# Kernel tuning notes

Hardware: AMD Instinct MI355X
Metric: run time of the kernel (lower is better)

## Reference

```python
import jax, jax.numpy as jnp
import numpy as np

N_NODES = 100000
N_EDGES = 600000
D_IN = 128
D_OUT = 128


def setup_inputs() -> dict:
    key = jax.random.key(0)
    ks = jax.random.split(key, 8)
    stdv = 1.0 / np.sqrt(D_OUT)
    return {
        "x": jax.random.normal(ks[0], (N_NODES, D_IN), dtype=jnp.float32),
        "edge_src": jax.random.randint(ks[1], (N_EDGES,), 0, N_NODES, dtype=jnp.int32),
        "edge_dst": jax.random.randint(ks[2], (N_EDGES,), 0, N_NODES, dtype=jnp.int32),
        "edge_weight": jax.random.uniform(ks[3], (N_EDGES,), dtype=jnp.float32),
        "weight_l": jax.random.uniform(ks[4], (D_IN, D_OUT), minval=-stdv, maxval=stdv, dtype=jnp.float32),
        "bias_l": jax.random.uniform(ks[5], (D_OUT,), minval=-stdv, maxval=stdv, dtype=jnp.float32),
        "weight_r": jax.random.uniform(ks[6], (D_IN, D_OUT), minval=-stdv, maxval=stdv, dtype=jnp.float32),
        "bias_r": jax.random.uniform(ks[7], (D_OUT,), minval=-stdv, maxval=stdv, dtype=jnp.float32),
    }


def reference(x, edge_src, edge_dst, edge_weight, weight_l, bias_l, weight_r, bias_r):
    # h = input @ weight_l  -> [N, D_OUT]
    h = x @ weight_l
    # spmm(adj, h): out[dst] += adj[dst, src] * h[src]
    msgs = h[edge_src] * edge_weight[:, None]          # [E, D_OUT] gather
    agg = jax.ops.segment_sum(msgs, edge_dst, num_segments=N_NODES)
    out = agg + bias_l
    # root_weight branch (size is None)
    out = out + x @ weight_r + bias_r
    return out
```

## Files before the change

kernel.cpp:

```cpp
#include <hip/hip_runtime.h>
#include <hip/hip_bf16.h>

#define D 128
#define SCAN_BLK 256
#define SCAN_VPT 4
#define SCAN_TILE (SCAN_BLK * SCAN_VPT)

typedef __attribute__((ext_vector_type(8))) short short8;
typedef __attribute__((ext_vector_type(4))) float f32x4;

__global__ __launch_bounds__(256) void prep_w(
    const float* __restrict__ Wl, const float* __restrict__ Wr,
    const float* __restrict__ bl, const float* __restrict__ br,
    __hip_bfloat16* __restrict__ WTl, __hip_bfloat16* __restrict__ WTr,
    float* __restrict__ bsum) {
  const int tid = blockIdx.x * 256 + threadIdx.x;
  const int n = (tid >> 7) & 127;
  const int k = tid & 127;
  if (tid < 16384) {
    WTl[n * D + k] = __float2bfloat16(Wl[k * D + n]);
  } else {
    WTr[n * D + k] = __float2bfloat16(Wr[k * D + n]);
  }
  if (tid < 128) bsum[tid] = bl[tid] + br[tid];
}

__global__ __launch_bounds__(256) void gemm_h(
    const float* __restrict__ x, const __hip_bfloat16* __restrict__ WTl,
    __hip_bfloat16* __restrict__ h,
    const int* __restrict__ edst, int* __restrict__ deg, int n_edges,
    int n_rowtiles) {
  const int gsz = gridDim.x * 256;
  for (int e = blockIdx.x * 256 + threadIdx.x; e < n_edges; e += gsz)
    atomicAdd(&deg[edst[e]], 1);

  __shared__ __hip_bfloat16 xs[16][136];
  const int t = threadIdx.x;
  const int wave = t >> 6;
  const int lane = t & 63;
  const int m = lane & 15;
  const int q = lane >> 4;

  short8 bfrag[2][4];
#pragma unroll
  for (int c = 0; c < 2; ++c) {
    const int n0 = wave * 32 + c * 16;
#pragma unroll
    for (int ks = 0; ks < 4; ++ks)
      bfrag[c][ks] = *(const short8*)&WTl[(n0 + m) * D + ks * 32 + q * 8];
  }

  const int srow = t >> 4;
  const int scol = (t & 15) * 8;

  for (int rt = blockIdx.x; rt < n_rowtiles; rt += gridDim.x) {
    const int rowbase = rt * 16;
    {
      const float4* src = (const float4*)&x[(size_t)(rowbase + srow) * D + scol];
      const float4 v0 = src[0], v1 = src[1];
      __hip_bfloat16* dst = &xs[srow][scol];
      dst[0] = __float2bfloat16(v0.x); dst[1] = __float2bfloat16(v0.y);
      dst[2] = __float2bfloat16(v0.z); dst[3] = __float2bfloat16(v0.w);
      dst[4] = __float2bfloat16(v1.x); dst[5] = __float2bfloat16(v1.y);
      dst[6] = __float2bfloat16(v1.z); dst[7] = __float2bfloat16(v1.w);
    }
    __syncthreads();

    f32x4 acc[2];
#pragma unroll
    for (int c = 0; c < 2; ++c)
#pragma unroll
      for (int r = 0; r < 4; ++r) acc[c][r] = 0.f;

#pragma unroll
    for (int ks = 0; ks < 4; ++ks) {
      const short8 afrag = *(const short8*)&xs[m][ks * 32 + q * 8];
#pragma unroll
      for (int c = 0; c < 2; ++c)
        acc[c] = __builtin_amdgcn_mfma_f32_16x16x32_bf16(afrag, bfrag[c][ks], acc[c], 0, 0, 0);
    }

#pragma unroll
    for (int c = 0; c < 2; ++c) {
      const int n = wave * 32 + c * 16 + m;
#pragma unroll
      for (int r = 0; r < 4; ++r)
        h[(size_t)(rowbase + q * 4 + r) * D + n] = __float2bfloat16(acc[c][r]);
    }
    __syncthreads();
  }
}

__global__ __launch_bounds__(SCAN_BLK) void scan1_kernel(
    const int* __restrict__ deg, int* __restrict__ offsets,
    int* __restrict__ partials, int n) {
  __shared__ int sdata[SCAN_BLK];
  const int t = threadIdx.x;
  const int base = blockIdx.x * SCAN_TILE + t * SCAN_VPT;

  int v[SCAN_VPT];
  int s = 0;
#pragma unroll
  for (int j = 0; j < SCAN_VPT; ++j) {
    v[j] = (base + j < n) ? deg[base + j] : 0;
    s += v[j];
  }
  sdata[t] = s;
  __syncthreads();
  for (int off = 1; off < SCAN_BLK; off <<= 1) {
    int xv = (t >= off) ? sdata[t - off] : 0;
    __syncthreads();
    sdata[t] += xv;
    __syncthreads();
  }
  int excl = sdata[t] - s;
  if (t == SCAN_BLK - 1) partials[blockIdx.x] = sdata[t];
  int run = excl;
#pragma unroll
  for (int j = 0; j < SCAN_VPT; ++j) {
    if (base + j < n) offsets[base + j] = run;
    run += v[j];
  }
}

__global__ __launch_bounds__(SCAN_BLK) void scan3_kernel(
    int* __restrict__ offsets, int* __restrict__ pos,
    const int* __restrict__ partials, int n, int n_edges) {
  __shared__ int s_add;
  const int t = threadIdx.x;
  if (t < 64) {
    int v = 0;
    for (int j = t; j < blockIdx.x; j += 64) v += partials[j];
#pragma unroll
    for (int off = 32; off > 0; off >>= 1) v += __shfl_down(v, off);
    if (t == 0) s_add = v;
  }
  __syncthreads();
  const int add = s_add;
  const int base = blockIdx.x * SCAN_TILE + t * SCAN_VPT;
#pragma unroll
  for (int j = 0; j < SCAN_VPT; ++j) {
    const int i = base + j;
    if (i < n) {
      const int o = offsets[i] + add;
      offsets[i] = o;
      pos[i] = o;
    }
  }
  if (blockIdx.x == 0 && t == 0) offsets[n] = n_edges;
}

__global__ __launch_bounds__(256) void scatter_kernel(
    const int* __restrict__ esrc, const int* __restrict__ edst,
    const float* __restrict__ ew, int* __restrict__ pos,
    int2* __restrict__ pairs, int n_edges) {
  const int e = blockIdx.x * 256 + threadIdx.x;
  if (e >= n_edges) return;
  const int d = edst[e];
  const int slot = atomicAdd(&pos[d], 1);
  pairs[slot] = make_int2(esrc[e], __float_as_int(ew[e]));
}

__global__ __launch_bounds__(256) void sage_out(
    const float* __restrict__ x, const __hip_bfloat16* __restrict__ WTr,
    const float* __restrict__ bsum, const __hip_bfloat16* __restrict__ h,
    const int* __restrict__ offsets, const int2* __restrict__ pairs,
    float* __restrict__ out) {
  __shared__ __hip_bfloat16 xs[16][136];
  __shared__ float ot[16][D];
  const int t = threadIdx.x;
  const int wave = t >> 6;
  const int lane = t & 63;
  const int m = lane & 15;
  const int q = lane >> 4;
  const int rowbase = blockIdx.x * 16;

  short8 bfrag[2][4];
#pragma unroll
  for (int c = 0; c < 2; ++c) {
    const int n0 = wave * 32 + c * 16;
#pragma unroll
    for (int ks = 0; ks < 4; ++ks)
      bfrag[c][ks] = *(const short8*)&WTr[(n0 + m) * D + ks * 32 + q * 8];
  }

  {
    const int srow = t >> 4;
    const int scol = (t & 15) * 8;
    const float4* src = (const float4*)&x[(size_t)(rowbase + srow) * D + scol];
    const float4 v0 = src[0], v1 = src[1];
    __hip_bfloat16* dst = &xs[srow][scol];
    dst[0] = __float2bfloat16(v0.x); dst[1] = __float2bfloat16(v0.y);
    dst[2] = __float2bfloat16(v0.z); dst[3] = __float2bfloat16(v0.w);
    dst[4] = __float2bfloat16(v1.x); dst[5] = __float2bfloat16(v1.y);
    dst[6] = __float2bfloat16(v1.z); dst[7] = __float2bfloat16(v1.w);
  }
  __syncthreads();

  f32x4 acc[2];
#pragma unroll
  for (int c = 0; c < 2; ++c)
#pragma unroll
    for (int r = 0; r < 4; ++r) acc[c][r] = 0.f;

#pragma unroll
  for (int ks = 0; ks < 4; ++ks) {
    const short8 afrag = *(const short8*)&xs[m][ks * 32 + q * 8];
#pragma unroll
    for (int c = 0; c < 2; ++c)
      acc[c] = __builtin_amdgcn_mfma_f32_16x16x32_bf16(afrag, bfrag[c][ks], acc[c], 0, 0, 0);
  }

#pragma unroll
  for (int c = 0; c < 2; ++c) {
    const int n = wave * 32 + c * 16 + m;
    const float b = bsum[n];
#pragma unroll
    for (int r = 0; r < 4; ++r)
      ot[q * 4 + r][n] = acc[c][r] + b;
  }
  __syncthreads();

  const __hip_bfloat162* __restrict__ h2 = (const __hip_bfloat162*)h;
#pragma unroll
  for (int j = 0; j < 4; ++j) {
    const int ln = wave * 4 + j;
    const int node = rowbase + ln;
    const int begin = offsets[node];
    const int end = offsets[node + 1];

    float2 a = *(const float2*)&ot[ln][2 * lane];

    int i = begin;
    for (; i + 4 <= end; i += 4) {
      const int2 p0 = pairs[i + 0];
      const int2 p1 = pairs[i + 1];
      const int2 p2 = pairs[i + 2];
      const int2 p3 = pairs[i + 3];
      const __hip_bfloat162 a0 = h2[(size_t)p0.x * (D / 2) + lane];
      const __hip_bfloat162 a1 = h2[(size_t)p1.x * (D / 2) + lane];
      const __hip_bfloat162 a2 = h2[(size_t)p2.x * (D / 2) + lane];
      const __hip_bfloat162 a3 = h2[(size_t)p3.x * (D / 2) + lane];
      const float w0 = __int_as_float(p0.y), w1 = __int_as_float(p1.y);
      const float w2 = __int_as_float(p2.y), w3 = __int_as_float(p3.y);
      a.x = fmaf(w0, __bfloat162float(a0.x), a.x);
      a.y = fmaf(w0, __bfloat162float(a0.y), a.y);
      a.x = fmaf(w1, __bfloat162float(a1.x), a.x);
      a.y = fmaf(w1, __bfloat162float(a1.y), a.y);
      a.x = fmaf(w2, __bfloat162float(a2.x), a.x);
      a.y = fmaf(w2, __bfloat162float(a2.y), a.y);
      a.x = fmaf(w3, __bfloat162float(a3.x), a.x);
      a.y = fmaf(w3, __bfloat162float(a3.y), a.y);
    }
    for (; i < end; ++i) {
      const int2 p = pairs[i];
      const __hip_bfloat162 av = h2[(size_t)p.x * (D / 2) + lane];
      const float w = __int_as_float(p.y);
      a.x = fmaf(w, __bfloat162float(av.x), a.x);
      a.y = fmaf(w, __bfloat162float(av.y), a.y);
    }
    *(float2*)&out[(size_t)node * D + 2 * lane] = a;
  }
}

extern "C" void kernel_launch(void* const* d_in, const int* in_sizes, int n_in,
                              void* d_out, int out_size, void* d_ws, size_t ws_size,
                              hipStream_t stream) {
  const float* x   = (const float*)d_in[0];
  const int* esrc  = (const int*)d_in[1];
  const int* edst  = (const int*)d_in[2];
  const float* ew  = (const float*)d_in[3];
  const float* Wl  = (const float*)d_in[4];
  const float* bl  = (const float*)d_in[5];
  const float* Wr  = (const float*)d_in[6];
  const float* br  = (const float*)d_in[7];
  float* out = (float*)d_out;

  const int n_nodes = in_sizes[0] / D;
  const int n_edges = in_sizes[1];

  char* ws = (char*)d_ws;
  size_t off = 0;
  __hip_bfloat16* h = (__hip_bfloat16*)(ws + off);
  off += (size_t)n_nodes * D * sizeof(__hip_bfloat16);
  off = (off + 15) & ~15ull;
  int* offsets = (int*)(ws + off);
  off += (size_t)(n_nodes + 1) * sizeof(int);
  off = (off + 15) & ~15ull;
  int* pos = (int*)(ws + off);
  off += (size_t)n_nodes * sizeof(int);
  off = (off + 15) & ~15ull;
  int* partials = (int*)(ws + off);
  off += 1024 * sizeof(int);
  off = (off + 15) & ~15ull;
  int2* pairs = (int2*)(ws + off);
  off += (size_t)n_edges * sizeof(int2);
  off = (off + 15) & ~15ull;
  __hip_bfloat16* WTl = (__hip_bfloat16*)(ws + off);
  off += (size_t)D * D * sizeof(__hip_bfloat16);
  __hip_bfloat16* WTr = (__hip_bfloat16*)(ws + off);
  off += (size_t)D * D * sizeof(__hip_bfloat16);
  float* bsum = (float*)(ws + off);
  off += D * sizeof(float);

  const int n_rowtiles = (n_nodes + 15) / 16;

  hipMemsetAsync(pos, 0, (size_t)n_nodes * sizeof(int), stream);
  prep_w<<<128, 256, 0, stream>>>(Wl, Wr, bl, br, WTl, WTr, bsum);

  const int gemm_grid = n_rowtiles < 2048 ? n_rowtiles : 2048;
  gemm_h<<<gemm_grid, 256, 0, stream>>>(x, WTl, h, edst, pos, n_edges, n_rowtiles);

  const int nparts = (n_nodes + SCAN_TILE - 1) / SCAN_TILE;
  scan1_kernel<<<nparts, SCAN_BLK, 0, stream>>>(pos, offsets, partials, n_nodes);
  scan3_kernel<<<nparts, SCAN_BLK, 0, stream>>>(offsets, pos, partials, n_nodes, n_edges);
  scatter_kernel<<<(n_edges + 255) / 256, 256, 0, stream>>>(esrc, edst, ew, pos, pairs, n_edges);

  sage_out<<<n_rowtiles, 256, 0, stream>>>(x, WTr, bsum, h, offsets, pairs, out);
}
```

Baseline: 236.9 us.

## Stage block's neighbor rows into LDS with cooperative gathers issued before the GEMM

The sage_out kernel now gathers the h rows of all edges belonging to its 16-node block cooperatively into shared memory, in chunks of 112 edges. Each thread loads 64 bytes of a row with int4 loads, and the first chunk's loads are issued before the x@Wr MFMA section so their latency overlaps with the GEMM. Each wave then accumulates its 4 nodes from LDS and adds the root/bias term at the end. This replaces the per-wave serial 4-byte-per-lane gathers with wider, more parallel memory requests. In exchange it uses about 30KB of LDS, adds extra barriers for high-degree blocks, and sets a launch-bounds occupancy hint of 4.

```diff
diff --git a/kernel.cpp b/kernel.cpp
--- a/kernel.cpp
+++ b/kernel.cpp
@@ -5,6 +5,9 @@
 #define SCAN_BLK 256
 #define SCAN_VPT 4
 #define SCAN_TILE (SCAN_BLK * SCAN_VPT)
+
+#define KC 112
+#define HROW 272
 
 typedef __attribute__((ext_vector_type(8))) short short8;
 typedef __attribute__((ext_vector_type(4))) float f32x4;
@@ -161,13 +164,16 @@
   pairs[slot] = make_int2(esrc[e], __float_as_int(ew[e]));
 }
 
-__global__ __launch_bounds__(256) void sage_out(
+__global__ __launch_bounds__(256, 4) void sage_out(
     const float* __restrict__ x, const __hip_bfloat16* __restrict__ WTr,
     const float* __restrict__ bsum, const __hip_bfloat16* __restrict__ h,
     const int* __restrict__ offsets, const int2* __restrict__ pairs,
     float* __restrict__ out) {
-  __shared__ __hip_bfloat16 xs[16][136];
   __shared__ float ot[16][D];
+  __shared__ float wbuf[KC];
+  __shared__ __align__(16) char Hbuf[KC * HROW];
+  __hip_bfloat16 (*xs)[136] = reinterpret_cast<__hip_bfloat16(*)[136]>(Hbuf);
+
   const int t = threadIdx.x;
   const int wave = t >> 6;
   const int lane = t & 63;
@@ -175,6 +181,36 @@
   const int q = lane >> 4;
   const int rowbase = blockIdx.x * 16;
 
+  const int gB0 = offsets[rowbase];
+  const int Eb = offsets[rowbase + 16] - gB0;
+  int nb[4], ne[4];
+#pragma unroll
+  for (int j = 0; j < 4; ++j) {
+    nb[j] = offsets[rowbase + wave * 4 + j] - gB0;
+    ne[j] = offsets[rowbase + wave * 4 + j + 1] - gB0;
+  }
+
+  const int cnt0 = Eb < KC ? Eb : KC;
+  const int le0 = t >> 2;
+  const int le1 = (t + 256) >> 2;
+  const int qt = t & 3;
+  const bool v0 = le0 < cnt0;
+  const bool v1 = le1 < cnt0;
+  int2 pr0 = make_int2(0, 0), pr1 = make_int2(0, 0);
+  int4 g0[4], g1[4];
+  if (v0) {
+    pr0 = pairs[gB0 + le0];
+    const int4* p = (const int4*)((const char*)h + ((size_t)(unsigned)pr0.x << 8) + (qt << 6));
+#pragma unroll
+    for (int i = 0; i < 4; ++i) g0[i] = p[i];
+  }
+  if (v1) {
+    pr1 = pairs[gB0 + le1];
+    const int4* p = (const int4*)((const char*)h + ((size_t)(unsigned)pr1.x << 8) + (qt << 6));
+#pragma unroll
+    for (int i = 0; i < 4; ++i) g1[i] = p[i];
+  }
+
   short8 bfrag[2][4];
 #pragma unroll
   for (int c = 0; c < 2; ++c) {
@@ -188,12 +224,12 @@
     const int srow = t >> 4;
     const int scol = (t & 15) * 8;
     const float4* src = (const float4*)&x[(size_t)(rowbase + srow) * D + scol];
-    const float4 v0 = src[0], v1 = src[1];
+    const float4 v0f = src[0], v1f = src[1];
     __hip_bfloat16* dst = &xs[srow][scol];
-    dst[0] = __float2bfloat16(v0.x); dst[1] = __float2bfloat16(v0.y);
-    dst[2] = __float2bfloat16(v0.z); dst[3] = __float2bfloat16(v0.w);
-    dst[4] = __float2bfloat16(v1.x); dst[5] = __float2bfloat16(v1.y);
-    dst[6] = __float2bfloat16(v1.z); dst[7] = __float2bfloat16(v1.w);
+    dst[0] = __float2bfloat16(v0f.x); dst[1] = __float2bfloat16(v0f.y);
+    dst[2] = __float2bfloat16(v0f.z); dst[3] = __float2bfloat16(v0f.w);
+    dst[4] = __float2bfloat16(v1f.x); dst[5] = __float2bfloat16(v1f.y);
+    dst[6] = __float2bfloat16(v1f.z); dst[7] = __float2bfloat16(v1f.w);
   }
   __syncthreads();
 
@@ -221,45 +257,75 @@
   }
   __syncthreads();
 
-  const __hip_bfloat162* __restrict__ h2 = (const __hip_bfloat162*)h;
+  float2 a[4];
+#pragma unroll
+  for (int j = 0; j < 4; ++j) a[j] = make_float2(0.f, 0.f);
+
+  for (int base = 0; base < Eb; base += KC) {
+    const int cnt = (Eb - base) < KC ? (Eb - base) : KC;
+    if (base == 0) {
+      if (v0) {
+        char* dst = &Hbuf[le0 * HROW + (qt << 6)];
+#pragma unroll
+        for (int i = 0; i < 4; ++i) ((int4*)dst)[i] = g0[i];
+        if (qt == 0) wbuf[le0] = __int_as_float(pr0.y);
+      }
+      if (v1) {
+        char* dst = &Hbuf[le1 * HROW + (qt << 6)];
+#pragma unroll
+        for (int i = 0; i < 4; ++i) ((int4*)dst)[i] = g1[i];
+        if (qt == 0) wbuf[le1] = __int_as_float(pr1.y);
+      }
+    } else {
+      __syncthreads();
+#pragma unroll
+      for (int s = 0; s < 2; ++s) {
+        const int le = (t + s * 256) >> 2;
+        if (le < cnt) {
+          const int2 pr = pairs[gB0 + base + le];
+          const int4* p = (const int4*)((const char*)h + ((size_t)(unsigned)pr.x << 8) + (qt << 6));
+          int4 g[4];
+#pragma unroll
+          for (int i = 0; i < 4; ++i) g[i] = p[i];
+          char* dst = &Hbuf[le * HROW + (qt << 6)];
+#pragma unroll
+          for (int i = 0; i < 4; ++i) ((int4*)dst)[i] = g[i];
+          if (qt == 0) wbuf[le] = __int_as_float(pr.y);
+        }
+      }
+    }
+    __syncthreads();
+
+#pragma unroll
+    for (int j = 0; j < 4; ++j) {
+      const int lo = nb[j] > base ? nb[j] : base;
+      const int hi0 = base + cnt;
+      const int hi = ne[j] < hi0 ? ne[j] : hi0;
+      if (lo < hi) {
+        int li = lo - base;
+        float w = wbuf[li];
+        __hip_bfloat162 hv = *(const __hip_bfloat162*)&Hbuf[li * HROW + lane * 4];
+        for (int i = lo + 1; i < hi; ++i) {
+          const int lj = i - base;
+          const float nw = wbuf[lj];
+          const __hip_bfloat162 nv = *(const __hip_bfloat162*)&Hbuf[lj * HROW + lane * 4];
+          a[j].x = fmaf(w, __bfloat162float(hv.x), a[j].x);
+          a[j].y = fmaf(w, __bfloat162float(hv.y), a[j].y);
+          w = nw; hv = nv;
+        }
+        a[j].x = fmaf(w, __bfloat162float(hv.x), a[j].x);
+        a[j].y = fmaf(w, __bfloat162float(hv.y), a[j].y);
+      }
+    }
+  }
+
 #pragma unroll
   for (int j = 0; j < 4; ++j) {
     const int ln = wave * 4 + j;
-    const int node = rowbase + ln;
-    const int begin = offsets[node];
-    const int end = offsets[node + 1];
-
-    float2 a = *(const float2*)&ot[ln][2 * lane];
-
-    int i = begin;
-    for (; i + 4 <= end; i += 4) {
-      const int2 p0 = pairs[i + 0];
-      const int2 p1 = pairs[i + 1];
-      const int2 p2 = pairs[i + 2];
-      const int2 p3 = pairs[i + 3];
-      const __hip_bfloat162 a0 = h2[(size_t)p0.x * (D / 2) + lane];
-      const __hip_bfloat162 a1 = h2[(size_t)p1.x * (D / 2) + lane];
-      const __hip_bfloat162 a2 = h2[(size_t)p2.x * (D / 2) + lane];
-      const __hip_bfloat162 a3 = h2[(size_t)p3.x * (D / 2) + lane];
-      const float w0 = __int_as_float(p0.y), w1 = __int_as_float(p1.y);
-      const float w2 = __int_as_float(p2.y), w3 = __int_as_float(p3.y);
-      a.x = fmaf(w0, __bfloat162float(a0.x), a.x);
-      a.y = fmaf(w0, __bfloat162float(a0.y), a.y);
-      a.x = fmaf(w1, __bfloat162float(a1.x), a.x);
-      a.y = fmaf(w1, __bfloat162float(a1.y), a.y);
-      a.x = fmaf(w2, __bfloat162float(a2.x), a.x);
-      a.y = fmaf(w2, __bfloat162float(a2.y), a.y);
-      a.x = fmaf(w3, __bfloat162float(a3.x), a.x);
-      a.y = fmaf(w3, __bfloat162float(a3.y), a.y);
-    }
-    for (; i < end; ++i) {
-      const int2 p = pairs[i];
-      const __hip_bfloat162 av = h2[(size_t)p.x * (D / 2) + lane];
-      const float w = __int_as_float(p.y);
-      a.x = fmaf(w, __bfloat162float(av.x), a.x);
-      a.y = fmaf(w, __bfloat162float(av.y), a.y);
-    }
-    *(float2*)&out[(size_t)node * D + 2 * lane] = a;
+    float2 o = *(const float2*)&ot[ln][2 * lane];
+    o.x += a[j].x;
+    o.y += a[j].y;
+    *(float2*)&out[(size_t)(rowbase + ln) * D + 2 * lane] = o;
   }
 }
 
```

Measured after the change: 269.8 us. 1.14x slower.

## Balance edge work across waves with shared-memory atomics and fold memset into prep

Applied to the files above, without the earlier changes.

Each block's edges for its 16 destination rows are now split evenly across the four waves instead of one wave per node. Each wave accumulates into a shared-memory output tile with LDS float atomics, using the local destination row packed into the high bits of the source index. This removes the load imbalance from skewed per-node degrees and unrolls gathers by 8. The separate memset is replaced by zeroing the degree array inside prep_w, saving one launch. The cost is LDS atomic contention, an interleaved column layout, and a limit on source indices of 24 bits.

```diff
diff --git a/kernel.cpp b/kernel.cpp
--- a/kernel.cpp
+++ b/kernel.cpp
@@ -13,7 +13,7 @@
     const float* __restrict__ Wl, const float* __restrict__ Wr,
     const float* __restrict__ bl, const float* __restrict__ br,
     __hip_bfloat16* __restrict__ WTl, __hip_bfloat16* __restrict__ WTr,
-    float* __restrict__ bsum) {
+    float* __restrict__ bsum, int* __restrict__ deg, int n_nodes) {
   const int tid = blockIdx.x * 256 + threadIdx.x;
   const int n = (tid >> 7) & 127;
   const int k = tid & 127;
@@ -23,6 +23,7 @@
     WTr[n * D + k] = __float2bfloat16(Wr[k * D + n]);
   }
   if (tid < 128) bsum[tid] = bl[tid] + br[tid];
+  for (int i = tid; i < n_nodes; i += 32768) deg[i] = 0;
 }
 
 __global__ __launch_bounds__(256) void gemm_h(
@@ -158,7 +159,7 @@
   if (e >= n_edges) return;
   const int d = edst[e];
   const int slot = atomicAdd(&pos[d], 1);
-  pairs[slot] = make_int2(esrc[e], __float_as_int(ew[e]));
+  pairs[slot] = make_int2(esrc[e] | ((d & 15) << 24), __float_as_int(ew[e]));
 }
 
 __global__ __launch_bounds__(256) void sage_out(
@@ -166,14 +167,21 @@
     const float* __restrict__ bsum, const __hip_bfloat16* __restrict__ h,
     const int* __restrict__ offsets, const int2* __restrict__ pairs,
     float* __restrict__ out) {
+  __shared__ float ot[16][D];
   __shared__ __hip_bfloat16 xs[16][136];
-  __shared__ float ot[16][D];
   const int t = threadIdx.x;
   const int wave = t >> 6;
   const int lane = t & 63;
   const int m = lane & 15;
   const int q = lane >> 4;
   const int rowbase = blockIdx.x * 16;
+
+  const int gB0 = offsets[rowbase];
+  const int Eb = offsets[rowbase + 16] - gB0;
+  int wb = gB0 + ((Eb * wave) >> 2);
+  int we = gB0 + ((Eb * (wave + 1)) >> 2);
+  wb = __builtin_amdgcn_readfirstlane(wb);
+  we = __builtin_amdgcn_readfirstlane(we);
 
   short8 bfrag[2][4];
 #pragma unroll
@@ -215,51 +223,50 @@
   for (int c = 0; c < 2; ++c) {
     const int n = wave * 32 + c * 16 + m;
     const float b = bsum[n];
+    const int slot = ((n & 1) << 6) | (n >> 1);
 #pragma unroll
     for (int r = 0; r < 4; ++r)
-      ot[q * 4 + r][n] = acc[c][r] + b;
+      ot[q * 4 + r][slot] = acc[c][r] + b;
   }
   __syncthreads();
 
   const __hip_bfloat162* __restrict__ h2 = (const __hip_bfloat162*)h;
+  float* __restrict__ otf = &ot[0][0];
+
+  int i = wb;
+  for (; i + 8 <= we; i += 8) {
+    int2 pr[8];
+#pragma unroll
+    for (int j = 0; j < 8; ++j) pr[j] = pairs[i + j];
+    __hip_bfloat162 hv[8];
+#pragma unroll
+    for (int j = 0; j < 8; ++j)
+      hv[j] = h2[(size_t)(pr[j].x & 0x00FFFFFF) * (D / 2) + lane];
+#pragma unroll
+    for (int j = 0; j < 8; ++j) {
+      const float w = __int_as_float(pr[j].y);
+      const int dl = ((unsigned)pr[j].x) >> 24;
+      atomicAdd(&otf[dl * D + lane], w * __bfloat162float(hv[j].x));
+      atomicAdd(&otf[dl * D + 64 + lane], w * __bfloat162float(hv[j].y));
+    }
+  }
+  for (; i < we; ++i) {
+    const int2 pr = pairs[i];
+    const __hip_bfloat162 hvs = h2[(size_t)(pr.x & 0x00FFFFFF) * (D / 2) + lane];
+    const float w = __int_as_float(pr.y);
+    const int dl = ((unsigned)pr.x) >> 24;
+    atomicAdd(&otf[dl * D + lane], w * __bfloat162float(hvs.x));
+    atomicAdd(&otf[dl * D + 64 + lane], w * __bfloat162float(hvs.y));
+  }
+  __syncthreads();
+
 #pragma unroll
   for (int j = 0; j < 4; ++j) {
     const int ln = wave * 4 + j;
-    const int node = rowbase + ln;
-    const int begin = offsets[node];
-    const int end = offsets[node + 1];
-
-    float2 a = *(const float2*)&ot[ln][2 * lane];
-
-    int i = begin;
-    for (; i + 4 <= end; i += 4) {
-      const int2 p0 = pairs[i + 0];
-      const int2 p1 = pairs[i + 1];
-      const int2 p2 = pairs[i + 2];
-      const int2 p3 = pairs[i + 3];
-      const __hip_bfloat162 a0 = h2[(size_t)p0.x * (D / 2) + lane];
-      const __hip_bfloat162 a1 = h2[(size_t)p1.x * (D / 2) + lane];
-      const __hip_bfloat162 a2 = h2[(size_t)p2.x * (D / 2) + lane];
-      const __hip_bfloat162 a3 = h2[(size_t)p3.x * (D / 2) + lane];
-      const float w0 = __int_as_float(p0.y), w1 = __int_as_float(p1.y);
-      const float w2 = __int_as_float(p2.y), w3 = __int_as_float(p3.y);
-      a.x = fmaf(w0, __bfloat162float(a0.x), a.x);
-      a.y = fmaf(w0, __bfloat162float(a0.y), a.y);
-      a.x = fmaf(w1, __bfloat162float(a1.x), a.x);
-      a.y = fmaf(w1, __bfloat162float(a1.y), a.y);
-      a.x = fmaf(w2, __bfloat162float(a2.x), a.x);
-      a.y = fmaf(w2, __bfloat162float(a2.y), a.y);
-      a.x = fmaf(w3, __bfloat162float(a3.x), a.x);
-      a.y = fmaf(w3, __bfloat162float(a3.y), a.y);
-    }
-    for (; i < end; ++i) {
-      const int2 p = pairs[i];
-      const __hip_bfloat162 av = h2[(size_t)p.x * (D / 2) + lane];
-      const float w = __int_as_float(p.y);
-      a.x = fmaf(w, __bfloat162float(av.x), a.x);
-      a.y = fmaf(w, __bfloat162float(av.y), a.y);
-    }
-    *(float2*)&out[(size_t)node * D + 2 * lane] = a;
+    float2 o;
+    o.x = ot[ln][lane];
+    o.y = ot[ln][64 + lane];
+    *(float2*)&out[(size_t)(rowbase + ln) * D + 2 * lane] = o;
   }
 }
 
@@ -305,8 +312,7 @@
 
   const int n_rowtiles = (n_nodes + 15) / 16;
 
-  hipMemsetAsync(pos, 0, (size_t)n_nodes * sizeof(int), stream);
-  prep_w<<<128, 256, 0, stream>>>(Wl, Wr, bl, br, WTl, WTr, bsum);
+  prep_w<<<128, 256, 0, stream>>>(Wl, Wr, bl, br, WTl, WTr, bsum, pos, n_nodes);
 
   const int gemm_grid = n_rowtiles < 2048 ? n_rowtiles : 2048;
   gemm_h<<<gemm_grid, 256, 0, stream>>>(x, WTl, h, edst, pos, n_edges, n_rowtiles);
```

After: 582.2 us. +145.8%, slower.

## Fuse scan and scatter into cooperative kernel, fold memset, unroll gather

Applied to the files above, without the earlier changes.

The two-pass degree scan and the edge scatter become one cooperative kernel that uses grid-wide syncs, so three separate launches turn into one. Zeroing the degree array moves from a memset into the weight-prep kernel. The neighbor gather loop in sage_out gains an 8-wide unrolled path so more h-row loads are in flight at once. In exchange, the code depends on a cooperative launch of 1024 resident blocks and pays for two grid barriers, and the scan chunk is smaller (128 nodes per block).

```diff
diff --git a/kernel.cpp b/kernel.cpp
--- a/kernel.cpp
+++ b/kernel.cpp
@@ -1,10 +1,12 @@
 #include <hip/hip_runtime.h>
 #include <hip/hip_bf16.h>
+#include <hip/hip_cooperative_groups.h>
+
+namespace cg = cooperative_groups;
 
 #define D 128
-#define SCAN_BLK 256
-#define SCAN_VPT 4
-#define SCAN_TILE (SCAN_BLK * SCAN_VPT)
+#define CS_BLOCKS 1024
+#define CS_CHUNK 128
 
 typedef __attribute__((ext_vector_type(8))) short short8;
 typedef __attribute__((ext_vector_type(4))) float f32x4;
@@ -13,7 +15,7 @@
     const float* __restrict__ Wl, const float* __restrict__ Wr,
     const float* __restrict__ bl, const float* __restrict__ br,
     __hip_bfloat16* __restrict__ WTl, __hip_bfloat16* __restrict__ WTr,
-    float* __restrict__ bsum) {
+    float* __restrict__ bsum, int* __restrict__ deg, int n_nodes) {
   const int tid = blockIdx.x * 256 + threadIdx.x;
   const int n = (tid >> 7) & 127;
   const int k = tid & 127;
@@ -23,6 +25,7 @@
     WTr[n * D + k] = __float2bfloat16(Wr[k * D + n]);
   }
   if (tid < 128) bsum[tid] = bl[tid] + br[tid];
+  for (int i = tid; i < n_nodes; i += 32768) deg[i] = 0;
 }
 
 __global__ __launch_bounds__(256) void gemm_h(
@@ -91,74 +94,61 @@
   }
 }
 
-__global__ __launch_bounds__(SCAN_BLK) void scan1_kernel(
-    const int* __restrict__ deg, int* __restrict__ offsets,
-    int* __restrict__ partials, int n) {
-  __shared__ int sdata[SCAN_BLK];
+__global__ __launch_bounds__(256) void coop_sort(
+    int* __restrict__ pos , int* __restrict__ offsets,
+    int* __restrict__ partials,
+    const int* __restrict__ esrc, const int* __restrict__ edst,
+    const float* __restrict__ ew, int2* __restrict__ pairs,
+    int n, int n_edges) {
+  cg::grid_group grid = cg::this_grid();
+  __shared__ int sdata[256];
+  __shared__ int s_add;
   const int t = threadIdx.x;
-  const int base = blockIdx.x * SCAN_TILE + t * SCAN_VPT;
-
-  int v[SCAN_VPT];
-  int s = 0;
-#pragma unroll
-  for (int j = 0; j < SCAN_VPT; ++j) {
-    v[j] = (base + j < n) ? deg[base + j] : 0;
-    s += v[j];
-  }
-  sdata[t] = s;
+  const int b = blockIdx.x;
+  const int base = b * CS_CHUNK;
+  const bool act = (t < CS_CHUNK) && (base + t < n);
+
+  int v = act ? pos[base + t] : 0;
+  sdata[t] = v;
   __syncthreads();
-  for (int off = 1; off < SCAN_BLK; off <<= 1) {
+  for (int off = 1; off < 256; off <<= 1) {
     int xv = (t >= off) ? sdata[t - off] : 0;
     __syncthreads();
     sdata[t] += xv;
     __syncthreads();
   }
-  int excl = sdata[t] - s;
-  if (t == SCAN_BLK - 1) partials[blockIdx.x] = sdata[t];
-  int run = excl;
-#pragma unroll
-  for (int j = 0; j < SCAN_VPT; ++j) {
-    if (base + j < n) offsets[base + j] = run;
-    run += v[j];
-  }
-}
-
-__global__ __launch_bounds__(SCAN_BLK) void scan3_kernel(
-    int* __restrict__ offsets, int* __restrict__ pos,
-    const int* __restrict__ partials, int n, int n_edges) {
-  __shared__ int s_add;
-  const int t = threadIdx.x;
+  const int excl = sdata[t] - v;
+  if (t == 255) partials[b] = sdata[t];
+  if (act) offsets[base + t] = excl;
+
+  __threadfence();
+  grid.sync();
+
   if (t < 64) {
-    int v = 0;
-    for (int j = t; j < blockIdx.x; j += 64) v += partials[j];
-#pragma unroll
-    for (int off = 32; off > 0; off >>= 1) v += __shfl_down(v, off);
-    if (t == 0) s_add = v;
+    int s = 0;
+    for (int j = t; j < b; j += 64) s += partials[j];
+#pragma unroll
+    for (int off = 32; off > 0; off >>= 1) s += __shfl_down(s, off);
+    if (t == 0) s_add = s;
   }
   __syncthreads();
   const int add = s_add;
-  const int base = blockIdx.x * SCAN_TILE + t * SCAN_VPT;
-#pragma unroll
-  for (int j = 0; j < SCAN_VPT; ++j) {
-    const int i = base + j;
-    if (i < n) {
-      const int o = offsets[i] + add;
-      offsets[i] = o;
-      pos[i] = o;
-    }
-  }
-  if (blockIdx.x == 0 && t == 0) offsets[n] = n_edges;
-}
-
-__global__ __launch_bounds__(256) void scatter_kernel(
-    const int* __restrict__ esrc, const int* __restrict__ edst,
-    const float* __restrict__ ew, int* __restrict__ pos,
-    int2* __restrict__ pairs, int n_edges) {
-  const int e = blockIdx.x * 256 + threadIdx.x;
-  if (e >= n_edges) return;
-  const int d = edst[e];
-  const int slot = atomicAdd(&pos[d], 1);
-  pairs[slot] = make_int2(esrc[e], __float_as_int(ew[e]));
+  if (act) {
+    const int o = offsets[base + t] + add;
+    offsets[base + t] = o;
+    pos[base + t] = o;
+  }
+  if (b == 0 && t == 0) offsets[n] = n_edges;
+
+  __threadfence();
+  grid.sync();
+
+  const int gsz = gridDim.x * 256;
+  for (int e = b * 256 + t; e < n_edges; e += gsz) {
+    const int d = edst[e];
+    const int slot = atomicAdd(&pos[d], 1);
+    pairs[slot] = make_int2(esrc[e], __float_as_int(ew[e]));
+  }
 }
 
 __global__ __launch_bounds__(256) void sage_out(
@@ -232,6 +222,21 @@
     float2 a = *(const float2*)&ot[ln][2 * lane];
 
     int i = begin;
+    for (; i + 8 <= end; i += 8) {
+      int2 p[8];
+#pragma unroll
+      for (int u = 0; u < 8; ++u) p[u] = pairs[i + u];
+      __hip_bfloat162 hv[8];
+#pragma unroll
+      for (int u = 0; u < 8; ++u)
+        hv[u] = h2[(size_t)p[u].x * (D / 2) + lane];
+#pragma unroll
+      for (int u = 0; u < 8; ++u) {
+        const float w = __int_as_float(p[u].y);
+        a.x = fmaf(w, __bfloat162float(hv[u].x), a.x);
+        a.y = fmaf(w, __bfloat162float(hv[u].y), a.y);
+      }
+    }
     for (; i + 4 <= end; i += 4) {
       const int2 p0 = pairs[i + 0];
       const int2 p1 = pairs[i + 1];
@@ -305,16 +310,19 @@
 
   const int n_rowtiles = (n_nodes + 15) / 16;
 
-  hipMemsetAsync(pos, 0, (size_t)n_nodes * sizeof(int), stream);
-  prep_w<<<128, 256, 0, stream>>>(Wl, Wr, bl, br, WTl, WTr, bsum);
+  prep_w<<<128, 256, 0, stream>>>(Wl, Wr, bl, br, WTl, WTr, bsum, pos, n_nodes);
 
   const int gemm_grid = n_rowtiles < 2048 ? n_rowtiles : 2048;
   gemm_h<<<gemm_grid, 256, 0, stream>>>(x, WTl, h, edst, pos, n_edges, n_rowtiles);
 
-  const int nparts = (n_nodes + SCAN_TILE - 1) / SCAN_TILE;
-  scan1_kernel<<<nparts, SCAN_BLK, 0, stream>>>(pos, offsets, partials, n_nodes);
-  scan3_kernel<<<nparts, SCAN_BLK, 0, stream>>>(offsets, pos, partials, n_nodes, n_edges);
-  scatter_kernel<<<(n_edges + 255) / 256, 256, 0, stream>>>(esrc, edst, ew, pos, pairs, n_edges);
+  {
+    int nn = n_nodes, ne = n_edges;
+    void* args[] = {(void*)&pos,  (void*)&offsets, (void*)&partials,
+                    (void*)&esrc, (void*)&edst,    (void*)&ew,
+                    (void*)&pairs, (void*)&nn,     (void*)&ne};
+    hipLaunchCooperativeKernel((void*)coop_sort, dim3(CS_BLOCKS), dim3(256),
+                               args, 0, stream);
+  }
 
   sage_out<<<n_rowtiles, 256, 0, stream>>>(x, WTr, bsum, h, offsets, pairs, out);
 }
```

After: 538.6 us. +127.3%, slower.
